# Kernel tuning notes

Measured on AMD Instinct MI355X. Metric: run time of the kernel, lower is better.

The kernel has to match this reference:

```python
import math
import jax, jax.numpy as jnp
import numpy as np

B, D, N, K = 16, 512, 2048, 32  # batch, latent_dim, n points, k feature width


def setup_inputs() -> dict:
    key = jax.random.key(0)
    ks = jax.random.split(key, 11)
    s = 0.02
    return {
        "x": jax.random.normal(ks[0], (B, D), jnp.float32),
        "WQ": jax.random.normal(ks[1], (D, N * K), jnp.float32) * s,
        "bQ": jax.random.normal(ks[2], (N * K,), jnp.float32) * s,
        "WK": jax.random.normal(ks[3], (D, N * K), jnp.float32) * s,
        "bK": jax.random.normal(ks[4], (N * K,), jnp.float32) * s,
        "WV": jax.random.normal(ks[5], (D, N * K), jnp.float32) * s,
        "bV": jax.random.normal(ks[6], (N * K,), jnp.float32) * s,
        "Wout": jax.random.normal(ks[7], (3, K), jnp.float32) * s,
        "bout": jax.random.normal(ks[8], (3,), jnp.float32) * s,
        "Wori": jax.random.normal(ks[9], (3, K), jnp.float32) * s,
        "bori": jax.random.normal(ks[10], (3,), jnp.float32) * s,
    }


def reference(x, WQ, bQ, WK, bK, WV, bV, Wout, bout, Wori, bori):
    b = x.shape[0]
    q = (x @ WQ + bQ).reshape(b, N, K)   # fc_Q output, used for both Q and ori
    k = (x @ WK + bK).reshape(b, N, K)
    v = (x @ WV + bV).reshape(b, N, K)
    # conv_ori is a pointwise Conv1d(K, 3, 1) applied to ori^T -> [b,3,N];
    # computed in [b,N,3] layout (final output layout after the last transpose).
    ori = jnp.einsum('bnk,ck->bnc', q, Wori) + bori  # [b, N, 3]
    # single-head scaled dot-product attention, scores [b, N, N]
    scores = jnp.einsum('bnk,bmk->bnm', q, k) / math.sqrt(K)
    attn = jax.nn.softmax(scores, axis=2)
    out = jnp.einsum('bnm,bmk->bnk', attn, v)        # [b, N, K]
    out = jnp.einsum('bnk,ck->bnc', out, Wout) + bout  # pointwise conv_output
    return out + ori                                 # [b, N, 3]
```

## Files before the change

kernel.cpp:

```cpp
#include <hip/hip_runtime.h>
#include <hip/hip_bf16.h>
#include <math.h>

#define NB 16
#define ND 512
#define NN 2048
#define NKF 32
#define NNK 65536

typedef short s8v __attribute__((ext_vector_type(8)));
typedef float f4v __attribute__((ext_vector_type(4)));
typedef unsigned short u16;
typedef unsigned int u32;
typedef u16 u16x8 __attribute__((ext_vector_type(8)));
typedef u32 u32x4 __attribute__((ext_vector_type(4)));

__device__ __forceinline__ u16 f2bf(float x) {
    u32 u = __builtin_bit_cast(u32, x);
    return (u16)((u + 0x7fffu + ((u >> 16) & 1u)) >> 16);
}
__device__ __forceinline__ float bf2f(u16 b) {
    u32 u = ((u32)b) << 16;
    return __builtin_bit_cast(float, u);
}

__global__ __launch_bounds__(256) void proj_partial(
    const float* __restrict__ x,
    const float* __restrict__ WQ, const float* __restrict__ WK,
    const float* __restrict__ WV, u16* __restrict__ part)
{
    const int t = threadIdx.x;
    const int jb = blockIdx.x;
    const int mat = blockIdx.y;
    const int dz = blockIdx.z;
    const float* __restrict__ W = (mat == 0) ? WQ : (mat == 1) ? WK : WV;
    const int j = jb * 1024 + t * 4;
    const int d0 = dz * 128;

    f4v acc[16];
    #pragma unroll
    for (int b = 0; b < 16; b++) acc[b] = (f4v){0.f, 0.f, 0.f, 0.f};

    const float* wp = W + (size_t)d0 * NNK + j;
    const float* xp = x + d0;

    f4v wa[8], wb[8];
    #pragma unroll
    for (int u = 0; u < 8; u++)
        wa[u] = __builtin_nontemporal_load((const f4v*)(wp + (size_t)u * NNK));

    #pragma unroll 1
    for (int dd = 0; dd < 128; dd += 16) {
        #pragma unroll
        for (int u = 0; u < 8; u++)
            wb[u] = __builtin_nontemporal_load(
                (const f4v*)(wp + (size_t)(dd + 8 + u) * NNK));
        __builtin_amdgcn_sched_barrier(0);

        #pragma unroll
        for (int u = 0; u < 8; u++) {
            const float* xr = xp + dd + u;
            #pragma unroll
            for (int b = 0; b < 16; b++) {
                float xv = xr[b * ND];
                acc[b][0] = fmaf(xv, wa[u][0], acc[b][0]);
                acc[b][1] = fmaf(xv, wa[u][1], acc[b][1]);
                acc[b][2] = fmaf(xv, wa[u][2], acc[b][2]);
                acc[b][3] = fmaf(xv, wa[u][3], acc[b][3]);
            }
        }

        if (dd + 16 < 128) {
            #pragma unroll
            for (int u = 0; u < 8; u++)
                wa[u] = __builtin_nontemporal_load(
                    (const f4v*)(wp + (size_t)(dd + 16 + u) * NNK));
        }
        __builtin_amdgcn_sched_barrier(0);

        #pragma unroll
        for (int u = 0; u < 8; u++) {
            const float* xr = xp + dd + 8 + u;
            #pragma unroll
            for (int b = 0; b < 16; b++) {
                float xv = xr[b * ND];
                acc[b][0] = fmaf(xv, wb[u][0], acc[b][0]);
                acc[b][1] = fmaf(xv, wb[u][1], acc[b][1]);
                acc[b][2] = fmaf(xv, wb[u][2], acc[b][2]);
                acc[b][3] = fmaf(xv, wb[u][3], acc[b][3]);
            }
        }
    }

    size_t base = ((size_t)(mat * 4 + dz) * 16) * NNK + j;
    #pragma unroll
    for (int b = 0; b < 16; b++) {
        u32 lo = (u32)f2bf(acc[b][0]) | ((u32)f2bf(acc[b][1]) << 16);
        u32 hi = (u32)f2bf(acc[b][2]) | ((u32)f2bf(acc[b][3]) << 16);
        *(uint2*)(part + base + (size_t)b * NNK) = make_uint2(lo, hi);
    }
}

__global__ __launch_bounds__(256) void reduce_cast(
    const u16* __restrict__ part,
    const float* __restrict__ bQ, const float* __restrict__ bK,
    const float* __restrict__ bV,
    u16* __restrict__ qb, u16* __restrict__ kb, u16* __restrict__ vT)
{
    const int t = threadIdx.x;
    const int jc = blockIdx.x;
    const int b  = blockIdx.y;
    const int mat = blockIdx.z;
    const float* __restrict__ bias = (mat == 0) ? bQ : (mat == 1) ? bK : bV;
    const int j = jc * 2048 + t * 8;

    float4 b0 = *(const float4*)(bias + j);
    float4 b1 = *(const float4*)(bias + j + 4);
    float v[8] = {b0.x, b0.y, b0.z, b0.w, b1.x, b1.y, b1.z, b1.w};

    #pragma unroll
    for (int dz = 0; dz < 4; dz++) {
        size_t p = ((size_t)(mat * 4 + dz) * 16 + b) * NNK + j;
        u16x8 pp = *(const u16x8*)(part + p);
        #pragma unroll
        for (int i = 0; i < 8; i++) v[i] += bf2f(pp[i]);
    }

    const float scale = (mat == 1) ? 0.2550868230023389f : 1.0f;
    u16 h[8];
    #pragma unroll
    for (int i = 0; i < 8; i++) h[i] = f2bf(v[i] * scale);

    __shared__ u16 vt[32][72];

    if (mat < 2) {
        u16* dst = ((mat == 0) ? qb : kb) + (size_t)b * NNK + j;
        u16x8 hv;
        #pragma unroll
        for (int i = 0; i < 8; i++) hv[i] = h[i];
        *(u16x8*)dst = hv;
    } else {
        const int n  = t >> 2;
        const int k0 = (t & 3) * 8;
        #pragma unroll
        for (int i = 0; i < 8; i++) vt[k0 + i][n] = h[i];
        __syncthreads();
        const int k  = t >> 3;
        const int c8 = t & 7;
        u16x8 ov;
        #pragma unroll
        for (int i = 0; i < 8; i++) ov[i] = vt[k][c8 * 8 + i];
        u16* dst = vT + (size_t)b * NNK + (size_t)k * NN + jc * 64 + c8 * 8;
        *(u16x8*)dst = ov;
    }
}

__global__ __launch_bounds__(256) void attn_kernel(
    const u16* __restrict__ qb, const u16* __restrict__ kb,
    const u16* __restrict__ vT,
    const float* __restrict__ Wout, const float* __restrict__ bout,
    const float* __restrict__ Wori, const float* __restrict__ bori,
    float* __restrict__ out)
{
    const int t = threadIdx.x;
    const int w = t >> 6;
    const int l = t & 63;
    const int g = l >> 4;
    const int n = l & 15;
    const int b = blockIdx.y;
    const int q0 = blockIdx.x * 64;

    __shared__ __align__(16) u16 Vs[2][2048];
    __shared__ __align__(16) u32 Pt[4][16][36];

    const u16* qrow = qb + (size_t)b * NNK + (size_t)(q0 + w * 16 + n) * NKF + g * 8;
    const s8v qf = *(const s8v*)qrow;

    const u16* kbase = kb + (size_t)b * NNK + (size_t)n * NKF + g * 8;
    auto loadK = [&](s8v (&ka)[4], int it) {
        #pragma unroll
        for (int tt = 0; tt < 4; tt++)
            ka[tt] = *(const s8v*)(kbase + (size_t)it * 2048 + tt * 512);
    };

    const int vrow = t >> 3, vslot = t & 7;
    const int vcolL = (vslot ^ (vrow & 7)) * 8;
    const u16* vgp = vT + (size_t)b * NNK + (size_t)vrow * NN + vcolL;

    s8v ka0[4], ka1[4], vreg;
    loadK(ka0, 0);
    vreg = *(const s8v*)(vgp);
    *(s8v*)(&Vs[0][t * 8]) = vreg;
    vreg = *(const s8v*)(vgp + 64);
    __syncthreads();

    float m_run = -INFINITY, l_run = 0.f;
    f4v O0 = {0.f, 0.f, 0.f, 0.f}, O1 = {0.f, 0.f, 0.f, 0.f};

    auto body = [&](s8v (&kc_)[4], s8v (&kn_)[4], int it) {
        const int cur = it & 1;
        if (it + 1 < 32) {
            *(s8v*)(&Vs[cur ^ 1][t * 8]) = vreg;
            loadK(kn_, it + 1);
        }
        if (it + 2 < 32)
            vreg = *(const s8v*)(vgp + (size_t)(it + 2) * 64);

        f4v S[4];
        #pragma unroll
        for (int tt = 0; tt < 4; tt++) {
            f4v z = {0.f, 0.f, 0.f, 0.f};
            S[tt] = __builtin_amdgcn_mfma_f32_16x16x32_bf16(kc_[tt], qf, z, 0, 0, 0);
        }

        float pmax = -INFINITY;
        #pragma unroll
        for (int tt = 0; tt < 4; tt++)
            #pragma unroll
            for (int r = 0; r < 4; r++) pmax = fmaxf(pmax, S[tt][r]);
        pmax = fmaxf(pmax, __shfl_xor(pmax, 16));
        pmax = fmaxf(pmax, __shfl_xor(pmax, 32));
        const float m_new = fmaxf(m_run, pmax);
        const float corr = exp2f(m_run - m_new);

        float p[4][4];
        float tsum = 0.f;
        #pragma unroll
        for (int tt = 0; tt < 4; tt++)
            #pragma unroll
            for (int r = 0; r < 4; r++) {
                p[tt][r] = exp2f(S[tt][r] - m_new);
                tsum += p[tt][r];
            }
        tsum += __shfl_xor(tsum, 16);
        tsum += __shfl_xor(tsum, 32);
        l_run = l_run * corr + tsum;
        m_run = m_new;
        #pragma unroll
        for (int r = 0; r < 4; r++) { O0[r] *= corr; O1[r] *= corr; }

        #pragma unroll
        for (int tt = 0; tt < 4; tt++) {
            u32 w0 = (u32)f2bf(p[tt][0]) | ((u32)f2bf(p[tt][1]) << 16);
            u32 w1 = (u32)f2bf(p[tt][2]) | ((u32)f2bf(p[tt][3]) << 16);
            *(uint2*)&Pt[w][n][8 * tt + 2 * g] = make_uint2(w0, w1);
        }

        #pragma unroll
        for (int kc = 0; kc < 2; kc++) {
            u32x4 pw = *(const u32x4*)&Pt[w][n][16 * kc + 4 * g];
            s8v pa = __builtin_bit_cast(s8v, pw);
            {
                int row = n;
                int slot = (g + 4 * kc) ^ (row & 7);
                s8v va = *(const s8v*)(&Vs[cur][row * 64 + slot * 8]);
                O0 = __builtin_amdgcn_mfma_f32_16x16x32_bf16(va, pa, O0, 0, 0, 0);
            }
            {
                int row = n + 16;
                int slot = (g + 4 * kc) ^ (row & 7);
                s8v va = *(const s8v*)(&Vs[cur][row * 64 + slot * 8]);
                O1 = __builtin_amdgcn_mfma_f32_16x16x32_bf16(va, pa, O1, 0, 0, 0);
            }
        }
        __syncthreads();
    };

    #pragma unroll 1
    for (int i2 = 0; i2 < 16; i2++) {
        body(ka0, ka1, 2 * i2);
        body(ka1, ka0, 2 * i2 + 1);
    }

    const float inv = 1.0f / l_run;
    float po[3] = {0.f, 0.f, 0.f};
    #pragma unroll
    for (int r = 0; r < 4; r++) {
        int dk0 = 4 * g + r;
        int dk1 = 16 + 4 * g + r;
        float o0 = O0[r] * inv;
        float o1 = O1[r] * inv;
        #pragma unroll
        for (int c = 0; c < 3; c++) {
            po[c] += o0 * Wout[c * NKF + dk0];
            po[c] += o1 * Wout[c * NKF + dk1];
        }
    }
    #pragma unroll
    for (int e = 0; e < 8; e++) {
        float qv = bf2f((u16)qf[e]);
        int k = 8 * g + e;
        #pragma unroll
        for (int c = 0; c < 3; c++) po[c] += qv * Wori[c * NKF + k];
    }
    #pragma unroll
    for (int c = 0; c < 3; c++) {
        po[c] += __shfl_xor(po[c], 16);
        po[c] += __shfl_xor(po[c], 32);
    }
    if (g == 0) {
        int row = q0 + w * 16 + n;
        size_t o = ((size_t)b * NN + row) * 3;
        #pragma unroll
        for (int c = 0; c < 3; c++) out[o + c] = po[c] + bout[c] + bori[c];
    }
}

extern "C" void kernel_launch(void* const* d_in, const int* in_sizes, int n_in,
                              void* d_out, int out_size, void* d_ws, size_t ws_size,
                              hipStream_t stream) {
    const float* x    = (const float*)d_in[0];
    const float* WQ   = (const float*)d_in[1];
    const float* bQ   = (const float*)d_in[2];
    const float* WK   = (const float*)d_in[3];
    const float* bK   = (const float*)d_in[4];
    const float* WV   = (const float*)d_in[5];
    const float* bV   = (const float*)d_in[6];
    const float* Wout = (const float*)d_in[7];
    const float* bout = (const float*)d_in[8];
    const float* Wori = (const float*)d_in[9];
    const float* bori = (const float*)d_in[10];
    float* out = (float*)d_out;

    char* ws = (char*)d_ws;
    u16* part = (u16*)ws;
    u16* qb = (u16*)(ws + 25165824);
    u16* kb = (u16*)(ws + 25165824 + 2097152);
    u16* vT = (u16*)(ws + 25165824 + 2 * 2097152);

    proj_partial<<<dim3(64, 3, 4), 256, 0, stream>>>(x, WQ, WK, WV, part);
    reduce_cast<<<dim3(32, 16, 3), 256, 0, stream>>>(part, bQ, bK, bV, qb, kb, vT);
    attn_kernel<<<dim3(32, 16), 256, 0, stream>>>(qb, kb, vT, Wout, bout, Wori, bori, out);
}
```

Measured before the change: 132.6 us.

## Load V fragments directly into registers instead of staging through LDS

Removes the shared-memory double buffer for the transposed V tile and the per-iteration block barrier. Each wave now loads its own V MFMA operands from global memory into registers, with register double-buffering alongside K. This cuts LDS traffic and __syncthreads stalls. In exchange, each of the 4 waves reads the same V data from global memory or L2 (4x redundant loads) and register pressure rises.

```diff
diff --git a/kernel.cpp b/kernel.cpp
--- a/kernel.cpp
+++ b/kernel.cpp
@@ -170,7 +170,6 @@
     const int b = blockIdx.y;
     const int q0 = blockIdx.x * 64;
 
-    __shared__ __align__(16) u16 Vs[2][2048];
     __shared__ __align__(16) u32 Pt[4][16][36];
 
     const u16* qrow = qb + (size_t)b * NNK + (size_t)(q0 + w * 16 + n) * NKF + g * 8;
@@ -182,29 +181,29 @@
         for (int tt = 0; tt < 4; tt++)
             ka[tt] = *(const s8v*)(kbase + (size_t)it * 2048 + tt * 512);
     };
-
-    const int vrow = t >> 3, vslot = t & 7;
-    const int vcolL = (vslot ^ (vrow & 7)) * 8;
-    const u16* vgp = vT + (size_t)b * NNK + (size_t)vrow * NN + vcolL;
-
-    s8v ka0[4], ka1[4], vreg;
+    const u16* vbase0 = vT + (size_t)b * NNK + (size_t)n * NN + g * 8;
+    const u16* vbase1 = vT + (size_t)b * NNK + (size_t)(n + 16) * NN + g * 8;
+    auto loadV = [&](s8v (&vf)[4], int it) {
+        const int off = it * 64;
+        vf[0] = *(const s8v*)(vbase0 + off);
+        vf[1] = *(const s8v*)(vbase0 + off + 32);
+        vf[2] = *(const s8v*)(vbase1 + off);
+        vf[3] = *(const s8v*)(vbase1 + off + 32);
+    };
+
+    s8v ka0[4], ka1[4], vf0[4], vf1[4];
     loadK(ka0, 0);
-    vreg = *(const s8v*)(vgp);
-    *(s8v*)(&Vs[0][t * 8]) = vreg;
-    vreg = *(const s8v*)(vgp + 64);
-    __syncthreads();
+    loadV(vf0, 0);
 
     float m_run = -INFINITY, l_run = 0.f;
     f4v O0 = {0.f, 0.f, 0.f, 0.f}, O1 = {0.f, 0.f, 0.f, 0.f};
 
-    auto body = [&](s8v (&kc_)[4], s8v (&kn_)[4], int it) {
-        const int cur = it & 1;
+    auto body = [&](s8v (&kc_)[4], s8v (&kn_)[4],
+                    s8v (&vc_)[4], s8v (&vn_)[4], int it) {
         if (it + 1 < 32) {
-            *(s8v*)(&Vs[cur ^ 1][t * 8]) = vreg;
             loadK(kn_, it + 1);
-        }
-        if (it + 2 < 32)
-            vreg = *(const s8v*)(vgp + (size_t)(it + 2) * 64);
+            loadV(vn_, it + 1);
+        }
 
         f4v S[4];
         #pragma unroll
@@ -250,26 +249,15 @@
         for (int kc = 0; kc < 2; kc++) {
             u32x4 pw = *(const u32x4*)&Pt[w][n][16 * kc + 4 * g];
             s8v pa = __builtin_bit_cast(s8v, pw);
-            {
-                int row = n;
-                int slot = (g + 4 * kc) ^ (row & 7);
-                s8v va = *(const s8v*)(&Vs[cur][row * 64 + slot * 8]);
-                O0 = __builtin_amdgcn_mfma_f32_16x16x32_bf16(va, pa, O0, 0, 0, 0);
-            }
-            {
-                int row = n + 16;
-                int slot = (g + 4 * kc) ^ (row & 7);
-                s8v va = *(const s8v*)(&Vs[cur][row * 64 + slot * 8]);
-                O1 = __builtin_amdgcn_mfma_f32_16x16x32_bf16(va, pa, O1, 0, 0, 0);
-            }
-        }
-        __syncthreads();
+            O0 = __builtin_amdgcn_mfma_f32_16x16x32_bf16(vc_[kc], pa, O0, 0, 0, 0);
+            O1 = __builtin_amdgcn_mfma_f32_16x16x32_bf16(vc_[2 + kc], pa, O1, 0, 0, 0);
+        }
     };
 
     #pragma unroll 1
     for (int i2 = 0; i2 < 16; i2++) {
-        body(ka0, ka1, 2 * i2);
-        body(ka1, ka0, 2 * i2 + 1);
+        body(ka0, ka1, vf0, vf1, 2 * i2);
+        body(ka1, ka0, vf1, vf0, 2 * i2 + 1);
     }
 
     const float inv = 1.0f / l_run;
```

Result: slower. 136.6 us (+3.0%).
